# Kernel optimization log

Measured on AMD Instinct MI355X. Metric: run time of the kernel, lower is better.

The kernel has to match this reference:

```python
import jax, jax.numpy as jnp
import numpy as np
from jax import lax

B, C, H, W = 8, 64, 128, 128
KS = 3          # kernel size
K = KS * KS     # kernel field = 9
PAD = 1


def conv2d(x, w, b):
    # x: [B,Cin,H,W], w: [Cout,Cin,kh,kw], 'same' 3x3 conv
    y = lax.conv_general_dilated(x, w, window_strides=(1, 1),
                                 padding=((PAD, PAD), (PAD, PAD)),
                                 dimension_numbers=('NCHW', 'OIHW', 'NCHW'))
    return y + b[None, :, None, None]


def modulated_deform_conv(x, offset, mask, weight, bias):
    # x:[B,C,H,W], offset:[B,2K,H,W] (dy,dx per tap), mask:[B,K,H,W]
    Bs, Cin, Hin, Win = x.shape
    off = offset.reshape(Bs, K, 2, Hin, Win)
    ky, kx = jnp.meshgrid(jnp.arange(KS), jnp.arange(KS), indexing='ij')
    ky = ky.reshape(K).astype(x.dtype)   # kernel tap row offsets 0..2
    kx = kx.reshape(K).astype(x.dtype)
    # sampling positions p = p0 + p_k + offset (stride=1, pad=1)
    py = (jnp.arange(Hin, dtype=x.dtype)[None, None, :, None] - PAD
          + ky[None, :, None, None] + off[:, :, 0])            # [B,K,H,W]
    px = (jnp.arange(Win, dtype=x.dtype)[None, None, None, :] - PAD
          + kx[None, :, None, None] + off[:, :, 1])            # [B,K,H,W]

    y0 = jnp.floor(py); x0 = jnp.floor(px)
    ly = py - y0; lx = px - x0                                  # frac parts
    y0i = y0.astype(jnp.int32); x0i = x0.astype(jnp.int32)

    x_flat = x.reshape(Bs, Cin, Hin * Win)

    def gather(iy, ix):
        valid = ((iy >= 0) & (iy < Hin) & (ix >= 0) & (ix < Win))
        flat = (jnp.clip(iy, 0, Hin - 1) * Win + jnp.clip(ix, 0, Win - 1))
        g = jax.vmap(lambda xb, ib: xb[:, ib])(x_flat, flat.reshape(Bs, -1))
        g = g.reshape(Bs, Cin, K, Hin, Win)
        return g * valid[:, None].astype(x.dtype)

    w00 = ((1 - ly) * (1 - lx))[:, None]  # [B,1,K,H,W]
    w01 = ((1 - ly) * lx)[:, None]
    w10 = (ly * (1 - lx))[:, None]
    w11 = (ly * lx)[:, None]

    val = (w00 * gather(y0i, x0i) + w01 * gather(y0i, x0i + 1)
           + w10 * gather(y0i + 1, x0i) + w11 * gather(y0i + 1, x0i + 1))
    val = val * mask[:, None]                                   # modulation
    out = jnp.einsum('ock,bckhw->bohw', weight.reshape(weight.shape[0], Cin, K), val)
    return out + bias[None, :, None, None]


def setup_inputs() -> dict:
    key = jax.random.key(0)
    ks = jax.random.split(key, 7)
    s = 0.05
    return {
        'x': jax.random.normal(ks[0], (B, C, H, W), jnp.float32),
        'w_om': jax.random.normal(ks[1], (3 * K, C, KS, KS), jnp.float32) * s,
        'b_om': jax.random.normal(ks[2], (3 * K,), jnp.float32) * s,
        'w_dc': jax.random.normal(ks[3], (C, C, KS, KS), jnp.float32) * s,
        'b_dc': jax.random.normal(ks[4], (C,), jnp.float32) * s,
        'w_c': jax.random.normal(ks[5], (C, C, KS, KS), jnp.float32) * s,
        'b_c': jax.random.normal(ks[6], (C,), jnp.float32) * s,
    }


def reference(x, w_om, b_om, w_dc, b_dc, w_c, b_c):
    om = conv2d(x, w_om, b_om)                       # [B,3K,H,W]
    offset, mask_raw = om[:, :2 * K], om[:, 2 * K:]
    mask = 2.0 * jax.nn.sigmoid(mask_raw)
    out = modulated_deform_conv(x, offset, mask, w_dc, b_dc)
    act = jnp.where(out > 0, out, 0.2 * out)         # LeakyReLU(0.2)
    return conv2d(act, w_c, b_c) + x
```

## Files before the change

kernel.cpp:

```cpp
#include <hip/hip_runtime.h>
#include <math.h>

#define Bn 8
#define Cn 64
#define Hn 128
#define Wn 128
#define HWn (Hn * Wn)

#define WOM_OFF 0
#define WDC_OFF 18432
#define WC_OFF 55296

typedef __attribute__((ext_vector_type(8))) short short8;
typedef __attribute__((ext_vector_type(4))) float floatx4;

__device__ __forceinline__ float bf2f(short s) {
  return __uint_as_float(((unsigned)(unsigned short)s) << 16);
}
__device__ __forceinline__ short f2bf(float f) {
  unsigned u = __float_as_uint(f);
  u += 0x7fff + ((u >> 16) & 1);
  return (short)(u >> 16);
}

__global__ __launch_bounds__(256) void k_prep_w(
    const float* __restrict__ w_om, const float* __restrict__ w_dc,
    const float* __restrict__ w_c, short* __restrict__ wt) {
  int idx = blockIdx.x * 256 + threadIdx.x;
  if (idx >= 92160) return;
  float v;
  if (idx < WDC_OFF) {
    int e = idx;
    int elem = e & 7, lane = (e >> 3) & 63, mt = (e >> 9) & 1, t = e >> 10;
    int kk = t % 9, cc = t / 9;
    int row = mt * 16 + (lane & 15);
    int cin = cc * 32 + (lane >> 4) * 8 + elem;
    v = (row < 27) ? w_om[(row * 64 + cin) * 9 + kk] : 0.f;
  } else {
    int e = (idx < WC_OFF) ? idx - WDC_OFF : idx - WC_OFF;
    const float* src = (idx < WC_OFF) ? w_dc : w_c;
    int elem = e & 7, lane = (e >> 3) & 63, mt = (e >> 9) & 3, t = e >> 11;
    int kk = t % 9, cc = t / 9;
    int row = mt * 16 + (lane & 15);
    int cin = cc * 32 + (lane >> 4) * 8 + elem;
    v = src[(row * 64 + cin) * 9 + kk];
  }
  wt[idx] = f2bf(v);
}

__global__ __launch_bounds__(256) void k_prep_x(const float* __restrict__ x,
                                                short* __restrict__ xT) {
  __shared__ float tile[64][129];
  const int bid = blockIdx.x;
  const int b = bid & 7, h = bid >> 3;
  const int tid = threadIdx.x;
  const float* xb = x + (size_t)b * 64 * HWn + h * Wn;
  for (int i = tid; i < 8192; i += 256) {
    int c = i >> 7, w = i & 127;
    tile[c][w] = xb[c * HWn + w];
  }
  __syncthreads();
  short* dst = xT + ((size_t)(b * Hn + h) * Wn) * 64;
  for (int i = tid; i < 2048; i += 256) {
    int w = i >> 4, c4 = (i & 15) * 4;
    short4 o;
    o.x = f2bf(tile[c4 + 0][w]);
    o.y = f2bf(tile[c4 + 1][w]);
    o.z = f2bf(tile[c4 + 2][w]);
    o.w = f2bf(tile[c4 + 3][w]);
    *(short4*)(dst + (size_t)w * 64 + c4) = o;
  }
}

__global__ __launch_bounds__(256, 4) void k_omdef(
    const short* __restrict__ xT, const short* __restrict__ wt,
    const float* __restrict__ b_om, const float* __restrict__ b_dc,
    short* __restrict__ actT) {
  __shared__ float som[27 * 66];
  __shared__ unsigned sbw[4 * 576];
  unsigned* sb01 = sbw;
  unsigned* sb23 = sbw + 576;
  unsigned* sw01 = sbw + 1152;
  unsigned* sw23 = sbw + 1728;

  const int bid = blockIdx.x;
  const int b = bid & 7;
  const int r = bid >> 3;
  const int h = r >> 1, w0 = (r & 1) * 64;
  const int tid = threadIdx.x;
  const int wave = tid >> 6, lane = tid & 63, quad = lane >> 4, lr = lane & 15;
  const short* xb = xT + (size_t)b * HWn * 64;
  const int pxl = wave * 16 + lr;
  const int gxp = w0 + pxl;

  floatx4 zf = {0.f, 0.f, 0.f, 0.f};

  floatx4 aco[2] = {zf, zf};
  for (int kk = 0; kk < 9; ++kk) {
    int ky = kk / 3, kx = kk - ky * 3;
    int gy = h + ky - 1, gx = gxp + kx - 1;
    bool ok = ((unsigned)gy < (unsigned)Hn) && ((unsigned)gx < (unsigned)Wn);
    int gyc = min(max(gy, 0), Hn - 1), gxc = min(max(gx, 0), Wn - 1);
    const short* rec = xb + (size_t)(gyc * Wn + gxc) * 64 + quad * 8;
#pragma unroll
    for (int cc = 0; cc < 2; ++cc) {
      short8 bf = *(const short8*)(rec + cc * 32);
      if (!ok) bf = (short8){0, 0, 0, 0, 0, 0, 0, 0};
      const short* ap = wt + WOM_OFF + (size_t)((cc * 9 + kk) * 2) * 512 + lane * 8;
      short8 a0 = *(const short8*)(ap);
      short8 a1 = *(const short8*)(ap + 512);
      aco[0] = __builtin_amdgcn_mfma_f32_16x16x32_bf16(a0, bf, aco[0], 0, 0, 0);
      aco[1] = __builtin_amdgcn_mfma_f32_16x16x32_bf16(a1, bf, aco[1], 0, 0, 0);
    }
  }
#pragma unroll
  for (int mt = 0; mt < 2; ++mt) {
#pragma unroll
    for (int rr = 0; rr < 4; ++rr) {
      int co = mt * 16 + quad * 4 + rr;
      if (co < 27) {
        float v = aco[mt][rr] + b_om[co];
        if (co >= 18) v = 2.f / (1.f + expf(-v));
        som[co * 66 + pxl] = v;
      }
    }
  }
  __syncthreads();

  for (int pr = tid; pr < 576; pr += 256) {
    int k = pr >> 6, p = pr & 63;
    float offy = som[(2 * k) * 66 + p];
    float offx = som[(2 * k + 1) * 66 + p];
    float m = som[(18 + k) * 66 + p];
    float py = (float)(h - 1 + (k / 3)) + offy;
    float px_ = (float)(w0 + p - 1 + (k % 3)) + offx;
    float fy = floorf(py), fx = floorf(px_);
    float ly = py - fy, lx = px_ - fx;
    int iy0 = (int)fy, ix0 = (int)fx;
    int iy1 = iy0 + 1, ix1 = ix0 + 1;
    bool vy0 = (iy0 >= 0) && (iy0 < Hn);
    bool vy1 = (iy1 >= 0) && (iy1 < Hn);
    bool vx0 = (ix0 >= 0) && (ix0 < Wn);
    bool vx1 = (ix1 >= 0) && (ix1 < Wn);
    unsigned cy0 = (unsigned)min(max(iy0, 0), Hn - 1);
    unsigned cy1 = (unsigned)min(max(iy1, 0), Hn - 1);
    unsigned cx0 = (unsigned)min(max(ix0, 0), Wn - 1);
    unsigned cx1 = (unsigned)min(max(ix1, 0), Wn - 1);
    sb01[pr] = (cy0 * Wn + cx0) | ((cy0 * Wn + cx1) << 16);
    sb23[pr] = (cy1 * Wn + cx0) | ((cy1 * Wn + cx1) << 16);
    float u0 = (vy0 && vx0) ? (1.f - ly) * (1.f - lx) * m : 0.f;
    float u1 = (vy0 && vx1) ? (1.f - ly) * lx * m : 0.f;
    float u2 = (vy1 && vx0) ? ly * (1.f - lx) * m : 0.f;
    float u3 = (vy1 && vx1) ? ly * lx * m : 0.f;
    sw01[pr] = (unsigned)(unsigned short)f2bf(u0) |
               ((unsigned)(unsigned short)f2bf(u1) << 16);
    sw23[pr] = (unsigned)(unsigned short)f2bf(u2) |
               ((unsigned)(unsigned short)f2bf(u3) << 16);
  }
  __syncthreads();

  floatx4 acc[4] = {zf, zf, zf, zf};
  for (int kk = 0; kk < 9; ++kk) {
    int pr = kk * 64 + pxl;
    unsigned a01 = sb01[pr], a23 = sb23[pr];
    unsigned uw01 = sw01[pr], uw23 = sw23[pr];
    float u0 = bf2f((short)(uw01 & 0xFFFF));
    float u1 = bf2f((short)(uw01 >> 16));
    float u2 = bf2f((short)(uw23 & 0xFFFF));
    float u3 = bf2f((short)(uw23 >> 16));
    const short* s0 = xb + (size_t)(a01 & 0xFFFF) * 64 + quad * 8;
    const short* s1 = xb + (size_t)(a01 >> 16) * 64 + quad * 8;
    const short* s2 = xb + (size_t)(a23 & 0xFFFF) * 64 + quad * 8;
    const short* s3 = xb + (size_t)(a23 >> 16) * 64 + quad * 8;
#pragma unroll
    for (int cc = 0; cc < 2; ++cc) {
      short8 q0 = *(const short8*)(s0 + cc * 32);
      short8 q1 = *(const short8*)(s1 + cc * 32);
      short8 q2 = *(const short8*)(s2 + cc * 32);
      short8 q3 = *(const short8*)(s3 + cc * 32);
      short8 bf;
#pragma unroll
      for (int e = 0; e < 8; ++e) {
        float f = u0 * bf2f(q0[e]) + u1 * bf2f(q1[e]) + u2 * bf2f(q2[e]) +
                  u3 * bf2f(q3[e]);
        bf[e] = f2bf(f);
      }
      const short* ap = wt + WDC_OFF + (size_t)((cc * 9 + kk) * 4) * 512 + lane * 8;
#pragma unroll
      for (int mt = 0; mt < 4; ++mt) {
        short8 am = *(const short8*)(ap + mt * 512);
        acc[mt] = __builtin_amdgcn_mfma_f32_16x16x32_bf16(am, bf, acc[mt], 0, 0, 0);
      }
    }
  }

  short* ab = actT + ((size_t)(b * Hn + h) * Wn + w0) * 64;
#pragma unroll
  for (int mt = 0; mt < 4; ++mt) {
    int c0 = mt * 16 + quad * 4;
    short4 o;
    float v;
    v = acc[mt][0] + b_dc[c0 + 0]; o.x = f2bf(v > 0.f ? v : 0.2f * v);
    v = acc[mt][1] + b_dc[c0 + 1]; o.y = f2bf(v > 0.f ? v : 0.2f * v);
    v = acc[mt][2] + b_dc[c0 + 2]; o.z = f2bf(v > 0.f ? v : 0.2f * v);
    v = acc[mt][3] + b_dc[c0 + 3]; o.w = f2bf(v > 0.f ? v : 0.2f * v);
    *(short4*)(ab + (size_t)pxl * 64 + c0) = o;
  }
}

__global__ __launch_bounds__(256, 4) void k_conv_out(
    const short* __restrict__ actT, const short* __restrict__ wt,
    const float* __restrict__ b_c, const float* __restrict__ x,
    float* __restrict__ out) {
  const int bid = blockIdx.x;
  const int b = bid & 7;
  const int r = bid >> 3;
  const int h = r >> 1, w0 = (r & 1) * 64;
  const int tid = threadIdx.x;
  const int wave = tid >> 6, lane = tid & 63, quad = lane >> 4, lr = lane & 15;
  const short* ab = actT + (size_t)b * HWn * 64;
  const int pxl = wave * 16 + lr;
  const int gxp = w0 + pxl;

  floatx4 zf = {0.f, 0.f, 0.f, 0.f};
  floatx4 acc[4] = {zf, zf, zf, zf};
  for (int kk = 0; kk < 9; ++kk) {
    int ky = kk / 3, kx = kk - ky * 3;
    int gy = h + ky - 1, gx = gxp + kx - 1;
    bool ok = ((unsigned)gy < (unsigned)Hn) && ((unsigned)gx < (unsigned)Wn);
    int gyc = min(max(gy, 0), Hn - 1), gxc = min(max(gx, 0), Wn - 1);
    const short* rec = ab + (size_t)(gyc * Wn + gxc) * 64 + quad * 8;
#pragma unroll
    for (int cc = 0; cc < 2; ++cc) {
      short8 bf = *(const short8*)(rec + cc * 32);
      if (!ok) bf = (short8){0, 0, 0, 0, 0, 0, 0, 0};
      const short* ap = wt + WC_OFF + (size_t)((cc * 9 + kk) * 4) * 512 + lane * 8;
#pragma unroll
      for (int mt = 0; mt < 4; ++mt) {
        short8 am = *(const short8*)(ap + mt * 512);
        acc[mt] = __builtin_amdgcn_mfma_f32_16x16x32_bf16(am, bf, acc[mt], 0, 0, 0);
      }
    }
  }

#pragma unroll
  for (int mt = 0; mt < 4; ++mt) {
#pragma unroll
    for (int rr = 0; rr < 4; ++rr) {
      int cout = mt * 16 + quad * 4 + rr;
      size_t gidx = ((size_t)(b * 64 + cout) * Hn + h) * Wn + w0 + pxl;
      out[gidx] = acc[mt][rr] + b_c[cout] + x[gidx];
    }
  }
}

extern "C" void kernel_launch(void* const* d_in, const int* in_sizes, int n_in,
                              void* d_out, int out_size, void* d_ws,
                              size_t ws_size, hipStream_t stream) {
  const float* x = (const float*)d_in[0];
  const float* w_om = (const float*)d_in[1];
  const float* b_om = (const float*)d_in[2];
  const float* w_dc = (const float*)d_in[3];
  const float* b_dc = (const float*)d_in[4];
  const float* w_c = (const float*)d_in[5];
  const float* b_c = (const float*)d_in[6];
  float* out = (float*)d_out;

  short* xT = (short*)d_ws;
  short* actT = xT + (size_t)Bn * HWn * 64;
  short* wt = actT + (size_t)Bn * HWn * 64;

  k_prep_w<<<dim3(360), 256, 0, stream>>>(w_om, w_dc, w_c, wt);
  k_prep_x<<<dim3(1024), 256, 0, stream>>>(x, xT);
  k_omdef<<<dim3(2048), 256, 0, stream>>>(xT, wt, b_om, b_dc, actT);
  k_conv_out<<<dim3(2048), 256, 0, stream>>>(actT, wt, b_c, x, out);
}
```

Before: 244.3 us.

## Stage conv weights in LDS and vectorize the residual output epilogue

Both fused kernels now copy the bf16 weight slices for each 32-channel half into a 36KB shared buffer and read MFMA A-operands from LDS instead of global memory. The loops are reordered so the channel half is outermost, which lets one slice be reused across all 9 taps. The output kernel also stages its accumulators through LDS so the residual add and store use coalesced 16-byte vector accesses. The change adds extra barriers and lowers the occupancy hint from 4 to 3 because of the larger LDS footprint.

```diff
diff --git a/kernel.cpp b/kernel.cpp
--- a/kernel.cpp
+++ b/kernel.cpp
@@ -72,10 +72,11 @@
   }
 }
 
-__global__ __launch_bounds__(256, 4) void k_omdef(
+__global__ __launch_bounds__(256, 3) void k_omdef(
     const short* __restrict__ xT, const short* __restrict__ wt,
     const float* __restrict__ b_om, const float* __restrict__ b_dc,
     short* __restrict__ actT) {
+  __shared__ __attribute__((aligned(16))) short lw[18432];
   __shared__ float som[27 * 66];
   __shared__ unsigned sbw[4 * 576];
   unsigned* sb01 = sbw;
@@ -95,7 +96,15 @@
 
   floatx4 zf = {0.f, 0.f, 0.f, 0.f};
 
+  {
+    const short8* src = (const short8*)(wt + WOM_OFF);
+    short8* dst = (short8*)lw;
+    for (int i = tid; i < 2304; i += 256) dst[i] = src[i];
+  }
+  __syncthreads();
+
   floatx4 aco[2] = {zf, zf};
+#pragma unroll 3
   for (int kk = 0; kk < 9; ++kk) {
     int ky = kk / 3, kx = kk - ky * 3;
     int gy = h + ky - 1, gx = gxp + kx - 1;
@@ -106,9 +115,8 @@
     for (int cc = 0; cc < 2; ++cc) {
       short8 bf = *(const short8*)(rec + cc * 32);
       if (!ok) bf = (short8){0, 0, 0, 0, 0, 0, 0, 0};
-      const short* ap = wt + WOM_OFF + (size_t)((cc * 9 + kk) * 2) * 512 + lane * 8;
-      short8 a0 = *(const short8*)(ap);
-      short8 a1 = *(const short8*)(ap + 512);
+      short8 a0 = *(const short8*)&lw[((cc * 9 + kk) * 2 + 0) * 512 + lane * 8];
+      short8 a1 = *(const short8*)&lw[((cc * 9 + kk) * 2 + 1) * 512 + lane * 8];
       aco[0] = __builtin_amdgcn_mfma_f32_16x16x32_bf16(a0, bf, aco[0], 0, 0, 0);
       aco[1] = __builtin_amdgcn_mfma_f32_16x16x32_bf16(a1, bf, aco[1], 0, 0, 0);
     }
@@ -127,6 +135,11 @@
   }
   __syncthreads();
 
+  {
+    const short8* src = (const short8*)(wt + WDC_OFF);
+    short8* dst = (short8*)lw;
+    for (int i = tid; i < 2304; i += 256) dst[i] = src[i];
+  }
   for (int pr = tid; pr < 576; pr += 256) {
     int k = pr >> 6, p = pr & 63;
     float offy = som[(2 * k) * 66 + p];
@@ -160,24 +173,28 @@
   __syncthreads();
 
   floatx4 acc[4] = {zf, zf, zf, zf};
-  for (int kk = 0; kk < 9; ++kk) {
-    int pr = kk * 64 + pxl;
-    unsigned a01 = sb01[pr], a23 = sb23[pr];
-    unsigned uw01 = sw01[pr], uw23 = sw23[pr];
-    float u0 = bf2f((short)(uw01 & 0xFFFF));
-    float u1 = bf2f((short)(uw01 >> 16));
-    float u2 = bf2f((short)(uw23 & 0xFFFF));
-    float u3 = bf2f((short)(uw23 >> 16));
-    const short* s0 = xb + (size_t)(a01 & 0xFFFF) * 64 + quad * 8;
-    const short* s1 = xb + (size_t)(a01 >> 16) * 64 + quad * 8;
-    const short* s2 = xb + (size_t)(a23 & 0xFFFF) * 64 + quad * 8;
-    const short* s3 = xb + (size_t)(a23 >> 16) * 64 + quad * 8;
-#pragma unroll
-    for (int cc = 0; cc < 2; ++cc) {
-      short8 q0 = *(const short8*)(s0 + cc * 32);
-      short8 q1 = *(const short8*)(s1 + cc * 32);
-      short8 q2 = *(const short8*)(s2 + cc * 32);
-      short8 q3 = *(const short8*)(s3 + cc * 32);
+  for (int cc = 0; cc < 2; ++cc) {
+    if (cc) {
+      __syncthreads();
+      const short8* src = (const short8*)(wt + WDC_OFF + 18432);
+      short8* dst = (short8*)lw;
+      for (int i = tid; i < 2304; i += 256) dst[i] = src[i];
+      __syncthreads();
+    }
+#pragma unroll 3
+    for (int kk = 0; kk < 9; ++kk) {
+      int pr = kk * 64 + pxl;
+      unsigned a01 = sb01[pr], a23 = sb23[pr];
+      unsigned uw01 = sw01[pr], uw23 = sw23[pr];
+      float u0 = bf2f((short)(uw01 & 0xFFFF));
+      float u1 = bf2f((short)(uw01 >> 16));
+      float u2 = bf2f((short)(uw23 & 0xFFFF));
+      float u3 = bf2f((short)(uw23 >> 16));
+      int co = cc * 32 + quad * 8;
+      short8 q0 = *(const short8*)(xb + (size_t)(a01 & 0xFFFF) * 64 + co);
+      short8 q1 = *(const short8*)(xb + (size_t)(a01 >> 16) * 64 + co);
+      short8 q2 = *(const short8*)(xb + (size_t)(a23 & 0xFFFF) * 64 + co);
+      short8 q3 = *(const short8*)(xb + (size_t)(a23 >> 16) * 64 + co);
       short8 bf;
 #pragma unroll
       for (int e = 0; e < 8; ++e) {
@@ -185,10 +202,9 @@
                   u3 * bf2f(q3[e]);
         bf[e] = f2bf(f);
       }
-      const short* ap = wt + WDC_OFF + (size_t)((cc * 9 + kk) * 4) * 512 + lane * 8;
 #pragma unroll
       for (int mt = 0; mt < 4; ++mt) {
-        short8 am = *(const short8*)(ap + mt * 512);
+        short8 am = *(const short8*)&lw[(kk * 4 + mt) * 512 + lane * 8];
         acc[mt] = __builtin_amdgcn_mfma_f32_16x16x32_bf16(am, bf, acc[mt], 0, 0, 0);
       }
     }
@@ -212,6 +228,8 @@
     const short* __restrict__ actT, const short* __restrict__ wt,
     const float* __restrict__ b_c, const float* __restrict__ x,
     float* __restrict__ out) {
+  __shared__ __attribute__((aligned(16))) short lw[18432];
+
   const int bid = blockIdx.x;
   const int b = bid & 7;
   const int r = bid >> 3;
@@ -224,33 +242,55 @@
 
   floatx4 zf = {0.f, 0.f, 0.f, 0.f};
   floatx4 acc[4] = {zf, zf, zf, zf};
-  for (int kk = 0; kk < 9; ++kk) {
-    int ky = kk / 3, kx = kk - ky * 3;
-    int gy = h + ky - 1, gx = gxp + kx - 1;
-    bool ok = ((unsigned)gy < (unsigned)Hn) && ((unsigned)gx < (unsigned)Wn);
-    int gyc = min(max(gy, 0), Hn - 1), gxc = min(max(gx, 0), Wn - 1);
-    const short* rec = ab + (size_t)(gyc * Wn + gxc) * 64 + quad * 8;
-#pragma unroll
-    for (int cc = 0; cc < 2; ++cc) {
-      short8 bf = *(const short8*)(rec + cc * 32);
+
+  for (int cc = 0; cc < 2; ++cc) {
+    if (cc) __syncthreads();
+    {
+      const short8* src = (const short8*)(wt + WC_OFF + cc * 18432);
+      short8* dst = (short8*)lw;
+      for (int i = tid; i < 2304; i += 256) dst[i] = src[i];
+    }
+    __syncthreads();
+#pragma unroll 3
+    for (int kk = 0; kk < 9; ++kk) {
+      int ky = kk / 3, kx = kk - ky * 3;
+      int gy = h + ky - 1, gx = gxp + kx - 1;
+      bool ok = ((unsigned)gy < (unsigned)Hn) && ((unsigned)gx < (unsigned)Wn);
+      int gyc = min(max(gy, 0), Hn - 1), gxc = min(max(gx, 0), Wn - 1);
+      short8 bf = *(const short8*)(ab + (size_t)(gyc * Wn + gxc) * 64 +
+                                   cc * 32 + quad * 8);
       if (!ok) bf = (short8){0, 0, 0, 0, 0, 0, 0, 0};
-      const short* ap = wt + WC_OFF + (size_t)((cc * 9 + kk) * 4) * 512 + lane * 8;
 #pragma unroll
       for (int mt = 0; mt < 4; ++mt) {
-        short8 am = *(const short8*)(ap + mt * 512);
+        short8 am = *(const short8*)&lw[(kk * 4 + mt) * 512 + lane * 8];
         acc[mt] = __builtin_amdgcn_mfma_f32_16x16x32_bf16(am, bf, acc[mt], 0, 0, 0);
       }
     }
   }
-
+  __syncthreads();
+
+  float* ot = (float*)lw;
 #pragma unroll
   for (int mt = 0; mt < 4; ++mt) {
 #pragma unroll
     for (int rr = 0; rr < 4; ++rr) {
-      int cout = mt * 16 + quad * 4 + rr;
-      size_t gidx = ((size_t)(b * 64 + cout) * Hn + h) * Wn + w0 + pxl;
-      out[gidx] = acc[mt][rr] + b_c[cout] + x[gidx];
-    }
+      ot[(mt * 16 + quad * 4 + rr) * 66 + pxl] = acc[mt][rr];
+    }
+  }
+  __syncthreads();
+
+  const int row = tid >> 2, seg = tid & 3;
+  const float bias = b_c[row];
+  const size_t gbase = ((size_t)(b * 64 + row) * Hn + h) * Wn + w0 + seg * 16;
+  const float* xr = x + gbase;
+  float* op = out + gbase;
+#pragma unroll
+  for (int j = 0; j < 4; ++j) {
+    floatx4 t = *(const floatx4*)&ot[row * 66 + seg * 16 + j * 4];
+    floatx4 xv = *(const floatx4*)&xr[j * 4];
+    t = t + xv;
+    t[0] += bias; t[1] += bias; t[2] += bias; t[3] += bias;
+    *(floatx4*)&op[j * 4] = t;
   }
 }
 
```

Measured after the change: 231.1 us. 5.4% less time.
